# Optimization experiments

Hardware: AMD Instinct MI355X
Metric: run time of the kernel (lower is better)

Reference implementation:

```python
import jax, jax.numpy as jnp
import numpy as np

# --- config (matches init_kwargs) ---
E = 32          # n_routed_experts
G = 8           # n_group
TKG = 4         # topk_group
K = 4           # num_experts_per_tok
D = 2048        # hidden_size
H = 1024        # moe_intermediate_size
HS = 4096       # moe_shared_expert_intermediate_size
SCALE = 2.5     # routed_scaling_factor
CAP = 1024


def setup_inputs() -> dict:
    key = jax.random.key(0)
    ks = jax.random.split(key, 6)
    B, S = 2, 2048
    return dict(
        hidden_states=jax.random.normal(ks[0], (B, S, D), jnp.float32),
        gate_w=jax.random.normal(ks[1], (E, D), jnp.float32) * 0.02,
        bias_corr=jnp.zeros((E,), jnp.float32),  # e_score_correction_bias
        up_w=jax.random.normal(ks[2], (E, H, D), jnp.float32) * 0.02,
        down_w=jax.random.normal(ks[3], (E, D, H), jnp.float32) * 0.02,
        shared_up_w=jax.random.normal(ks[4], (HS, D), jnp.float32) * 0.02,
        shared_down_w=jax.random.normal(ks[5], (D, HS), jnp.float32) * 0.02,
    )


def relu2(x):
    r = jnp.maximum(x, 0.0)
    return r * r


def route_tokens(scores, bias_corr):
    # scores: sigmoid(router_logits), [T, E]
    T = scores.shape[0]
    scores_c = scores + bias_corr                                  # for choice
    group_scores = jax.lax.top_k(scores_c.reshape(T, G, E // G), 2)[0].sum(-1)  # [T, G]
    _, group_idx = jax.lax.top_k(group_scores, TKG)                # [T, TKG]
    group_mask = jnp.zeros((T, G), scores.dtype).at[jnp.arange(T)[:, None], group_idx].set(1.0)
    score_mask = jnp.repeat(group_mask, E // G, axis=1)            # [T, E]
    masked = jnp.where(score_mask > 0, scores_c, 0.0)
    _, topk_idx = jax.lax.top_k(masked, K)                         # [T, K]
    topk_w = jnp.take_along_axis(scores, topk_idx, axis=1)         # weights from raw sigmoid scores
    topk_w = topk_w / (topk_w.sum(-1, keepdims=True) + 1e-20)      # norm_topk_prob
    return topk_idx, topk_w * SCALE


def reference(hidden_states, gate_w, bias_corr, up_w, down_w, shared_up_w, shared_down_w):
    B, S, _ = hidden_states.shape
    T = B * S
    flat = hidden_states.reshape(T, D)

    logits = flat @ gate_w.T                                       # [T, E]
    scores = jax.nn.sigmoid(logits)
    topk_idx, topk_w = route_tokens(scores, bias_corr)             # [T, K] each

    # --- capacity-based dispatch (equivalent to per-expert gather + index_add combine) ---
    e_flat = topk_idx.reshape(-1)                                  # [T*K]
    oh = jax.nn.one_hot(e_flat, E, dtype=jnp.int32)                # [T*K, E]
    pos = jnp.take_along_axis(jnp.cumsum(oh, axis=0) - 1, e_flat[:, None], axis=1)[:, 0]
    tok = jnp.repeat(jnp.arange(T), K)                             # token idx per assignment
    valid = pos < CAP

    xe = jnp.zeros((E, CAP, D), flat.dtype).at[e_flat, pos].set(flat[tok], mode='drop')
    h = relu2(jnp.einsum('ecd,ehd->ech', xe, up_w))                # [E, CAP, H]
    ye = jnp.einsum('ech,edh->ecd', h, down_w)                     # [E, CAP, D]

    gathered = ye[e_flat, jnp.minimum(pos, CAP - 1)]               # [T*K, D]
    gathered = jnp.where(valid[:, None], gathered, 0.0) * topk_w.reshape(-1)[:, None]
    routed = gathered.reshape(T, K, D).sum(axis=1).reshape(B, S, D)

    shared = relu2(hidden_states @ shared_up_w.T) @ shared_down_w.T
    return routed + shared
```

## Files before the change

### kernel.cpp

```cpp
#include <hip/hip_runtime.h>

#define NE 32
#define NG 8
#define NK 4
#define ND 2048
#define NH 1024
#define NHS 4096
#define CAPE 1024
#define NT 4096

typedef float f32x4 __attribute__((ext_vector_type(4)));
typedef short s16x8 __attribute__((ext_vector_type(8)));

__device__ __forceinline__ short f2bf(float f) {
    return __builtin_bit_cast(short, (__bf16)f);
}
__device__ __forceinline__ float bf2f(short h) {
    return __builtin_bit_cast(float, ((unsigned)(unsigned short)h) << 16);
}

__device__ __forceinline__ void gload_lds16(const void* g, void* l) {
    __builtin_amdgcn_global_load_lds(
        (const __attribute__((address_space(1))) void*)g,
        (__attribute__((address_space(3))) void*)l, 16, 0, 0);
}

__global__ __launch_bounds__(256) void gate_kernel(
    const float* __restrict__ X, const float* __restrict__ Gw,
    const float* __restrict__ bias,
    int* __restrict__ topk_idx, float* __restrict__ topk_w)
{
    const int lane = threadIdx.x & 63;
    const int t = blockIdx.x * 4 + (threadIdx.x >> 6);
    const float* x = X + (size_t)t * ND;

    float xr[32];
#pragma unroll
    for (int i = 0; i < 32; i++) xr[i] = x[lane + i * 64];

    float scores[32];
#pragma unroll
    for (int e = 0; e < 32; e++) {
        const float* w = Gw + (size_t)e * ND;
        float a = 0.f;
#pragma unroll
        for (int i = 0; i < 32; i++) a = fmaf(xr[i], w[lane + i * 64], a);
#pragma unroll
        for (int s = 32; s > 0; s >>= 1) a += __shfl_xor(a, s);
        scores[e] = 1.0f / (1.0f + expf(-a));
    }

    float sc_c[32];
#pragma unroll
    for (int e = 0; e < 32; e++) sc_c[e] = scores[e] + bias[e];

    float gs[8];
#pragma unroll
    for (int g = 0; g < 8; g++) {
        float a = sc_c[4 * g], b = sc_c[4 * g + 1], c = sc_c[4 * g + 2], d = sc_c[4 * g + 3];
        float hi1 = fmaxf(a, b), lo1 = fminf(a, b);
        float hi2 = fmaxf(c, d), lo2 = fminf(c, d);
        float m1 = fmaxf(hi1, hi2);
        float m2 = fmaxf(fminf(hi1, hi2), fmaxf(lo1, lo2));
        gs[g] = m1 + m2;
    }

    unsigned gsel = 0;
#pragma unroll
    for (int it = 0; it < 4; it++) {
        int best = -1; float bv = -1e30f;
#pragma unroll
        for (int g = 0; g < 8; g++) {
            bool avail = !((gsel >> g) & 1);
            if (avail && gs[g] > bv) { bv = gs[g]; best = g; }
        }
        gsel |= 1u << best;
    }

    unsigned esel = 0;
    int idxs[4]; float wts[4];
#pragma unroll
    for (int it = 0; it < 4; it++) {
        int best = -1; float bv = -1e30f, braw = 0.f;
#pragma unroll
        for (int e = 0; e < 32; e++) {
            float mv = ((gsel >> (e >> 2)) & 1) ? sc_c[e] : 0.0f;
            bool avail = !((esel >> e) & 1);
            if (avail && mv > bv) { bv = mv; best = e; braw = scores[e]; }
        }
        esel |= 1u << best;
        idxs[it] = best; wts[it] = braw;
    }

    float s = wts[0] + wts[1] + wts[2] + wts[3] + 1e-20f;
    if (lane == 0) {
#pragma unroll
        for (int k = 0; k < 4; k++) {
            topk_idx[t * 4 + k] = idxs[k];
            topk_w[t * 4 + k] = wts[k] / s * 2.5f;
        }
    }
}

__global__ void zero_cnt(int* cnt) {
    if (threadIdx.x < NE) cnt[threadIdx.x] = 0;
}

__global__ void dispatch_kernel(const int* __restrict__ topk_idx,
                                int* __restrict__ cnt,
                                int* __restrict__ tok_list,
                                int* __restrict__ pos_list)
{
    int i = blockIdx.x * 256 + threadIdx.x;
    int e = topk_idx[i];
    int t = i >> 2;
    int pos = atomicAdd(&cnt[e], 1);
    pos_list[i] = pos;
    if (pos < CAPE) {
        tok_list[e * CAPE + pos] = t;
    }
}

__global__ __launch_bounds__(256) void cvt_f2bf(const float* __restrict__ in,
                                                short* __restrict__ out, int n8)
{
    int i = blockIdx.x * 256 + threadIdx.x;
    int stride = gridDim.x * 256;
    for (; i < n8; i += stride) {
        const f32x4* p = (const f32x4*)(in + (size_t)i * 8);
        f32x4 a = p[0], b = p[1];
        s16x8 h;
        h[0] = f2bf(a[0]); h[1] = f2bf(a[1]); h[2] = f2bf(a[2]); h[3] = f2bf(a[3]);
        h[4] = f2bf(b[0]); h[5] = f2bf(b[1]); h[6] = f2bf(b[2]); h[7] = f2bf(b[3]);
        *(s16x8*)(out + (size_t)i * 8) = h;
    }
}

__global__ __launch_bounds__(256) void combine_kernel(
    const int* __restrict__ topk_idx, const float* __restrict__ topk_w,
    const int* __restrict__ pos_list,
    const short* __restrict__ Ybuf, float* __restrict__ out)
{
    const int t = blockIdx.x;
    const int d0 = threadIdx.x * 8;

    int e[NK], p[NK]; float w[NK];
#pragma unroll
    for (int k = 0; k < NK; k++) {
        e[k] = topk_idx[t * NK + k];
        p[k] = pos_list[t * NK + k];
        w[k] = topk_w[t * NK + k];
    }

    float* orow = out + (size_t)t * ND + d0;
    f32x4 o0 = *(f32x4*)(orow);
    f32x4 o1 = *(f32x4*)(orow + 4);

#pragma unroll
    for (int k = 0; k < NK; k++) {
        if (p[k] < CAPE) {
            s16x8 y = *(const s16x8*)(Ybuf + ((size_t)e[k] * CAPE + p[k]) * ND + d0);
            o0[0] = fmaf(w[k], bf2f(y[0]), o0[0]);
            o0[1] = fmaf(w[k], bf2f(y[1]), o0[1]);
            o0[2] = fmaf(w[k], bf2f(y[2]), o0[2]);
            o0[3] = fmaf(w[k], bf2f(y[3]), o0[3]);
            o1[0] = fmaf(w[k], bf2f(y[4]), o1[0]);
            o1[1] = fmaf(w[k], bf2f(y[5]), o1[1]);
            o1[2] = fmaf(w[k], bf2f(y[6]), o1[2]);
            o1[3] = fmaf(w[k], bf2f(y[7]), o1[3]);
        }
    }
    *(f32x4*)(orow) = o0;
    *(f32x4*)(orow + 4) = o1;
}

template <int MODE>
__global__ __launch_bounds__(256, 2) void moe_gemm4(
    const short* __restrict__ Abase, const short* __restrict__ Bbase,
    const int* __restrict__ cnt, const int* __restrict__ tok_list,
    short* __restrict__ Hout, float* __restrict__ out)
{
    constexpr int K = (MODE == 0) ? ND : (MODE == 1) ? NH : (MODE == 2) ? ND : NHS;
    constexpr int NTILES = K / 64;

    const int e = blockIdx.z;
    const int m0 = blockIdx.y * 128, n0 = blockIdx.x * 128;

    int mcnt = 0;
    if constexpr (MODE == 0 || MODE == 1) {
        mcnt = min(cnt[e], CAPE);
        if (m0 >= mcnt) return;
    }

    __shared__ short As[2][128 * 64];
    __shared__ short Bs[2][128 * 64];

    const int tid = threadIdx.x;
    const int lane = tid & 63;
    const int wave = tid >> 6;
    const int wr = wave >> 1, wc = wave & 1;

    const short* Ab = Abase;
    const short* Bb = Bbase;
    if constexpr (MODE == 0) Bb += (size_t)e * NH * ND;
    if constexpr (MODE == 1) { Ab += (size_t)e * CAPE * NH; Bb += (size_t)e * ND * NH; }

    const int srow = tid >> 3;
    const int p = tid & 7;
    const int gcol = (p ^ (srow & 7)) * 8;
    const short* asrc[4];
    const short* bsrc[4];
    int dstoff[4];
#pragma unroll
    for (int o = 0; o < 4; o++) {
        int r = o * 32 + srow;
        if constexpr (MODE == 0) {
            int gr = min(m0 + r, mcnt - 1);
            int tok = tok_list[e * CAPE + gr];
            asrc[o] = Abase + (size_t)tok * ND + gcol;
        } else if constexpr (MODE == 1) {
            int gr = min(m0 + r, mcnt - 1);
            asrc[o] = Ab + (size_t)gr * NH + gcol;
        } else if constexpr (MODE == 2) {
            asrc[o] = Abase + (size_t)(m0 + r) * ND + gcol;
        } else {
            asrc[o] = Abase + (size_t)(m0 + r) * NHS + gcol;
        }
        bsrc[o] = Bb + (size_t)(n0 + o * 32 + srow) * K + gcol;
        dstoff[o] = o * 2048 + wave * 512;
    }

    auto STAGE = [&](int tt) {
        const int ko = (tt < NTILES ? tt : NTILES - 1) * 64;
        short* Ad = As[tt & 1];
        short* Bd = Bs[tt & 1];
#pragma unroll
        for (int o = 0; o < 4; o++) gload_lds16(asrc[o] + ko, Ad + dstoff[o]);
#pragma unroll
        for (int o = 0; o < 4; o++) gload_lds16(bsrc[o] + ko, Bd + dstoff[o]);
    };

    const int r16 = lane & 15;
    const int physbase = ((lane >> 4) ^ (lane & 7)) * 8;
    int offA[4], offB[4];
#pragma unroll
    for (int m = 0; m < 4; m++)
        offA[m] = (wr * 64 + m * 16 + r16) * 64 + physbase;
#pragma unroll
    for (int n = 0; n < 4; n++)
        offB[n] = (wc * 64 + n * 16 + r16) * 64 + physbase;

    f32x4 acc[4][4] = {};

    STAGE(0);
    STAGE(1);

    for (int t = 0; t < NTILES; ++t) {
        const short* At = As[t & 1];
        const short* Bt = Bs[t & 1];
        asm volatile("s_waitcnt vmcnt(8)" ::: "memory");
        __builtin_amdgcn_s_barrier();
        __builtin_amdgcn_sched_barrier(0);
        s16x8 af[4], bf[4];
#pragma unroll
        for (int m = 0; m < 4; m++) af[m] = *(const s16x8*)(At + offA[m]);
#pragma unroll
        for (int n = 0; n < 4; n++) bf[n] = *(const s16x8*)(Bt + offB[n]);
        asm volatile("s_waitcnt lgkmcnt(0)" ::: "memory");
        __builtin_amdgcn_sched_barrier(0);
        __builtin_amdgcn_s_setprio(1);
#pragma unroll
        for (int m = 0; m < 4; m++)
#pragma unroll
            for (int n = 0; n < 4; n++)
                acc[m][n] = __builtin_amdgcn_mfma_f32_16x16x32_bf16(af[m], bf[n], acc[m][n], 0, 0, 0);
        __builtin_amdgcn_s_setprio(0);
        s16x8 ag[4], bg[4];
#pragma unroll
        for (int m = 0; m < 4; m++) ag[m] = *(const s16x8*)(At + (offA[m] ^ 32));
#pragma unroll
        for (int n = 0; n < 4; n++) bg[n] = *(const s16x8*)(Bt + (offB[n] ^ 32));
        asm volatile("s_waitcnt lgkmcnt(0)" ::: "memory");
        __builtin_amdgcn_sched_barrier(0);
        __builtin_amdgcn_s_barrier();
        __builtin_amdgcn_sched_barrier(0);
        STAGE(t + 2);
        __builtin_amdgcn_s_setprio(1);
#pragma unroll
        for (int m = 0; m < 4; m++)
#pragma unroll
            for (int n = 0; n < 4; n++)
                acc[m][n] = __builtin_amdgcn_mfma_f32_16x16x32_bf16(ag[m], bg[n], acc[m][n], 0, 0, 0);
        __builtin_amdgcn_s_setprio(0);
    }

    const int r0 = (lane >> 4) * 4;
    const int cc = lane & 15;

    if constexpr (MODE == 0 || MODE == 2) {
#pragma unroll
        for (int i = 0; i < 4; i++)
#pragma unroll
            for (int j = 0; j < 4; j++)
#pragma unroll
                for (int v = 0; v < 4; v++) {
                    int row = wr * 64 + i * 16 + r0 + v;
                    int col = wc * 64 + j * 16 + cc;
                    float val = acc[i][j][v];
                    float r = fmaxf(val, 0.f);
                    val = r * r;
                    if constexpr (MODE == 0)
                        Hout[((size_t)e * CAPE + m0 + row) * NH + (n0 + col)] = f2bf(val);
                    else
                        Hout[(size_t)(m0 + row) * NHS + (n0 + col)] = f2bf(val);
                }
    } else if constexpr (MODE == 3) {
#pragma unroll
        for (int i = 0; i < 4; i++)
#pragma unroll
            for (int j = 0; j < 4; j++)
#pragma unroll
                for (int v = 0; v < 4; v++) {
                    int row = wr * 64 + i * 16 + r0 + v;
                    int col = wc * 64 + j * 16 + cc;
                    out[(size_t)(m0 + row) * ND + (n0 + col)] = acc[i][j][v];
                }
    } else {
#pragma unroll
        for (int i = 0; i < 4; i++)
#pragma unroll
            for (int v = 0; v < 4; v++) {
                int row = wr * 64 + i * 16 + r0 + v;
                int grow = m0 + row;
                if (grow < mcnt) {
#pragma unroll
                    for (int j = 0; j < 4; j++) {
                        int col = wc * 64 + j * 16 + cc;
                        Hout[((size_t)e * CAPE + grow) * ND + (n0 + col)] = f2bf(acc[i][j][v]);
                    }
                }
            }
    }
}

extern "C" void kernel_launch(void* const* d_in, const int* in_sizes, int n_in,
                              void* d_out, int out_size, void* d_ws, size_t ws_size,
                              hipStream_t stream) {
    const float* X    = (const float*)d_in[0];
    const float* Gw   = (const float*)d_in[1];
    const float* bias = (const float*)d_in[2];
    const float* up_w = (const float*)d_in[3];
    const float* dn_w = (const float*)d_in[4];
    const float* sup  = (const float*)d_in[5];
    const float* sdn  = (const float*)d_in[6];
    float* out = (float*)d_out;

    char* ws = (char*)d_ws;
    size_t off = 0;
    auto alloc = [&](size_t bytes) -> void* {
        off = (off + 255) & ~(size_t)255;
        void* p = ws + off;
        off += bytes;
        return p;
    };
    int*   cnt      = (int*)  alloc(NE * 4);
    int*   topk_idx = (int*)  alloc((size_t)NT * NK * 4);
    float* topk_w   = (float*)alloc((size_t)NT * NK * 4);
    int*   pos_list = (int*)  alloc((size_t)NT * NK * 4);
    int*   tok_list = (int*)  alloc((size_t)NE * CAPE * 4);
    short* Hbuf     = (short*)alloc((size_t)NE * CAPE * NH * 2);
    short* Sbuf     = (short*)alloc((size_t)NT * NHS * 2);
    short* Xbf      = (short*)alloc((size_t)NT * ND * 2);
    short* up_bf    = (short*)alloc((size_t)NE * NH * ND * 2);
    short* dn_bf    = (short*)alloc((size_t)NE * ND * NH * 2);
    short* sup_bf   = (short*)alloc((size_t)NHS * ND * 2);
    short* sdn_bf   = (short*)alloc((size_t)ND * NHS * 2);
    short* Ybuf     = Xbf;

    gate_kernel<<<dim3(NT / 4), dim3(256), 0, stream>>>(X, Gw, bias, topk_idx, topk_w);
    zero_cnt<<<dim3(1), dim3(64), 0, stream>>>(cnt);
    dispatch_kernel<<<dim3(NT * NK / 256), dim3(256), 0, stream>>>(
        topk_idx, cnt, tok_list, pos_list);

    cvt_f2bf<<<dim3(1024), dim3(256), 0, stream>>>(X,    Xbf,    NT * ND / 8);
    cvt_f2bf<<<dim3(2048), dim3(256), 0, stream>>>(up_w, up_bf,  NE * NH * ND / 8);
    cvt_f2bf<<<dim3(2048), dim3(256), 0, stream>>>(dn_w, dn_bf,  NE * ND * NH / 8);
    cvt_f2bf<<<dim3(1024), dim3(256), 0, stream>>>(sup,  sup_bf, NHS * ND / 8);
    cvt_f2bf<<<dim3(1024), dim3(256), 0, stream>>>(sdn,  sdn_bf, ND * NHS / 8);

    moe_gemm4<0><<<dim3(NH / 128, CAPE / 128, NE), dim3(256), 0, stream>>>(
        Xbf, up_bf, cnt, tok_list, Hbuf, nullptr);
    moe_gemm4<2><<<dim3(NHS / 128, NT / 128, 1), dim3(256), 0, stream>>>(
        Xbf, sup_bf, nullptr, nullptr, Sbuf, nullptr);
    moe_gemm4<3><<<dim3(ND / 128, NT / 128, 1), dim3(256), 0, stream>>>(
        Sbuf, sdn_bf, nullptr, nullptr, nullptr, out);
    moe_gemm4<1><<<dim3(ND / 128, CAPE / 128, NE), dim3(256), 0, stream>>>(
        Hbuf, dn_bf, cnt, tok_list, Ybuf, nullptr);
    combine_kernel<<<dim3(NT), dim3(256), 0, stream>>>(
        topk_idx, topk_w, pos_list, Ybuf, out);
}
```

Measured before the change: 678.5 us.

## Fuse fp32-to-bf16 weight conversion into GEMM B-tile loading

Removes the separate weight conversion kernels and has each GEMM load fp32 weight tiles through registers, converting to bf16 and writing them swizzled into LDS. The loop is unrolled by two with register double-buffering of B and prefetching three tiles ahead. This removes a large read/write pass over all weights, at the cost of doubled per-tile B traffic, extra VGPRs, and losing direct global-to-LDS loads for B. Ybuf now gets its own workspace instead of aliasing the bf16 X buffer.

Measured after the change: 645.0 us. 1.05x faster.

```diff
diff --git a/kernel.cpp b/kernel.cpp
--- a/kernel.cpp
+++ b/kernel.cpp
@@ -176,7 +176,7 @@
 
 template <int MODE>
 __global__ __launch_bounds__(256, 2) void moe_gemm4(
-    const short* __restrict__ Abase, const short* __restrict__ Bbase,
+    const short* __restrict__ Abase, const float* __restrict__ Bbase,
     const int* __restrict__ cnt, const int* __restrict__ tok_list,
     short* __restrict__ Hout, float* __restrict__ out)
 {
@@ -201,43 +201,65 @@
     const int wr = wave >> 1, wc = wave & 1;
 
     const short* Ab = Abase;
-    const short* Bb = Bbase;
+    const float* Bb = Bbase;
     if constexpr (MODE == 0) Bb += (size_t)e * NH * ND;
     if constexpr (MODE == 1) { Ab += (size_t)e * CAPE * NH; Bb += (size_t)e * ND * NH; }
 
     const int srow = tid >> 3;
-    const int p = tid & 7;
-    const int gcol = (p ^ (srow & 7)) * 8;
+    const int pA = tid & 7;
+    const int gcolA = (pA ^ (srow & 7)) * 8;
     const short* asrc[4];
-    const short* bsrc[4];
-    int dstoff[4];
+    int dstA[4];
 #pragma unroll
     for (int o = 0; o < 4; o++) {
         int r = o * 32 + srow;
         if constexpr (MODE == 0) {
             int gr = min(m0 + r, mcnt - 1);
             int tok = tok_list[e * CAPE + gr];
-            asrc[o] = Abase + (size_t)tok * ND + gcol;
+            asrc[o] = Abase + (size_t)tok * ND + gcolA;
         } else if constexpr (MODE == 1) {
             int gr = min(m0 + r, mcnt - 1);
-            asrc[o] = Ab + (size_t)gr * NH + gcol;
+            asrc[o] = Ab + (size_t)gr * NH + gcolA;
         } else if constexpr (MODE == 2) {
-            asrc[o] = Abase + (size_t)(m0 + r) * ND + gcol;
+            asrc[o] = Abase + (size_t)(m0 + r) * ND + gcolA;
         } else {
-            asrc[o] = Abase + (size_t)(m0 + r) * NHS + gcol;
-        }
-        bsrc[o] = Bb + (size_t)(n0 + o * 32 + srow) * K + gcol;
-        dstoff[o] = o * 2048 + wave * 512;
-    }
-
-    auto STAGE = [&](int tt) {
+            asrc[o] = Abase + (size_t)(m0 + r) * NHS + gcolA;
+        }
+        dstA[o] = o * 2048 + wave * 512;
+    }
+
+    const int brow = tid >> 4;
+    const int lc = tid & 15;
+    const float* bsrc[8];
+    int bdst[8];
+#pragma unroll
+    for (int o = 0; o < 8; o++) {
+        int r = o * 16 + brow;
+        bsrc[o] = Bb + (size_t)(n0 + r) * K + lc * 4;
+        int ks = lc >> 1;
+        bdst[o] = r * 64 + ((ks ^ (r & 7)) * 8) + (lc & 1) * 4;
+    }
+
+    auto STAGE_A = [&](int tt, int par) {
         const int ko = (tt < NTILES ? tt : NTILES - 1) * 64;
-        short* Ad = As[tt & 1];
-        short* Bd = Bs[tt & 1];
-#pragma unroll
-        for (int o = 0; o < 4; o++) gload_lds16(asrc[o] + ko, Ad + dstoff[o]);
-#pragma unroll
-        for (int o = 0; o < 4; o++) gload_lds16(bsrc[o] + ko, Bd + dstoff[o]);
+        short* Ad = As[par];
+#pragma unroll
+        for (int o = 0; o < 4; o++) gload_lds16(asrc[o] + ko, Ad + dstA[o]);
+    };
+    auto BLOAD = [&](int tt, f32x4* regs) {
+        const int ko = (tt < NTILES ? tt : NTILES - 1) * 64;
+#pragma unroll
+        for (int o = 0; o < 8; o++) regs[o] = *(const f32x4*)(bsrc[o] + ko);
+    };
+    auto BWRITE = [&](const f32x4* regs, int par) {
+        short* Bd = Bs[par];
+#pragma unroll
+        for (int o = 0; o < 8; o++) {
+            short4 h;
+            h.x = f2bf(regs[o][0]); h.y = f2bf(regs[o][1]);
+            h.z = f2bf(regs[o][2]); h.w = f2bf(regs[o][3]);
+            *(short4*)(Bd + bdst[o]) = h;
+        }
     };
 
     const int r16 = lane & 15;
@@ -251,48 +273,72 @@
         offB[n] = (wc * 64 + n * 16 + r16) * 64 + physbase;
 
     f32x4 acc[4][4] = {};
-
-    STAGE(0);
-    STAGE(1);
-
-    for (int t = 0; t < NTILES; ++t) {
-        const short* At = As[t & 1];
-        const short* Bt = Bs[t & 1];
-        asm volatile("s_waitcnt vmcnt(8)" ::: "memory");
-        __builtin_amdgcn_s_barrier();
-        __builtin_amdgcn_sched_barrier(0);
-        s16x8 af[4], bf[4];
-#pragma unroll
-        for (int m = 0; m < 4; m++) af[m] = *(const s16x8*)(At + offA[m]);
-#pragma unroll
-        for (int n = 0; n < 4; n++) bf[n] = *(const s16x8*)(Bt + offB[n]);
-        asm volatile("s_waitcnt lgkmcnt(0)" ::: "memory");
-        __builtin_amdgcn_sched_barrier(0);
-        __builtin_amdgcn_s_setprio(1);
-#pragma unroll
-        for (int m = 0; m < 4; m++)
-#pragma unroll
-            for (int n = 0; n < 4; n++)
-                acc[m][n] = __builtin_amdgcn_mfma_f32_16x16x32_bf16(af[m], bf[n], acc[m][n], 0, 0, 0);
-        __builtin_amdgcn_s_setprio(0);
-        s16x8 ag[4], bg[4];
-#pragma unroll
-        for (int m = 0; m < 4; m++) ag[m] = *(const s16x8*)(At + (offA[m] ^ 32));
-#pragma unroll
-        for (int n = 0; n < 4; n++) bg[n] = *(const s16x8*)(Bt + (offB[n] ^ 32));
-        asm volatile("s_waitcnt lgkmcnt(0)" ::: "memory");
-        __builtin_amdgcn_sched_barrier(0);
-        __builtin_amdgcn_s_barrier();
-        __builtin_amdgcn_sched_barrier(0);
-        STAGE(t + 2);
-        __builtin_amdgcn_s_setprio(1);
-#pragma unroll
-        for (int m = 0; m < 4; m++)
-#pragma unroll
-            for (int n = 0; n < 4; n++)
-                acc[m][n] = __builtin_amdgcn_mfma_f32_16x16x32_bf16(ag[m], bg[n], acc[m][n], 0, 0, 0);
-        __builtin_amdgcn_s_setprio(0);
-    }
+    f32x4 brE[8], brO[8];
+
+    STAGE_A(0, 0); STAGE_A(1, 1);
+    BLOAD(0, brE); BLOAD(1, brO);
+    asm volatile("s_waitcnt vmcnt(8)" ::: "memory");
+    __builtin_amdgcn_sched_barrier(0);
+    BWRITE(brE, 0);
+    asm volatile("s_waitcnt vmcnt(0)" ::: "memory");
+    __builtin_amdgcn_sched_barrier(0);
+    BWRITE(brO, 1);
+    BLOAD(2, brE);
+    asm volatile("s_waitcnt lgkmcnt(0)" ::: "memory");
+    __builtin_amdgcn_sched_barrier(0);
+
+#define GEMM_ITER(T, PAR, CONSUME, FILL)                                        \
+    {                                                                           \
+        __builtin_amdgcn_s_barrier();                                           \
+        __builtin_amdgcn_sched_barrier(0);                                      \
+        const short* At = As[PAR];                                              \
+        const short* Bt = Bs[PAR];                                              \
+        s16x8 af[4], bf[4];                                                     \
+        _Pragma("unroll")                                                       \
+        for (int m = 0; m < 4; m++) af[m] = *(const s16x8*)(At + offA[m]);      \
+        _Pragma("unroll")                                                       \
+        for (int n = 0; n < 4; n++) bf[n] = *(const s16x8*)(Bt + offB[n]);      \
+        asm volatile("s_waitcnt lgkmcnt(0)" ::: "memory");                      \
+        __builtin_amdgcn_sched_barrier(0);                                      \
+        __builtin_amdgcn_s_setprio(1);                                          \
+        _Pragma("unroll")                                                       \
+        for (int m = 0; m < 4; m++)                                             \
+            _Pragma("unroll")                                                   \
+            for (int n = 0; n < 4; n++)                                         \
+                acc[m][n] = __builtin_amdgcn_mfma_f32_16x16x32_bf16(            \
+                    af[m], bf[n], acc[m][n], 0, 0, 0);                          \
+        __builtin_amdgcn_s_setprio(0);                                          \
+        s16x8 ag[4], bg[4];                                                     \
+        _Pragma("unroll")                                                       \
+        for (int m = 0; m < 4; m++) ag[m] = *(const s16x8*)(At + (offA[m] ^ 32)); \
+        _Pragma("unroll")                                                       \
+        for (int n = 0; n < 4; n++) bg[n] = *(const s16x8*)(Bt + (offB[n] ^ 32)); \
+        asm volatile("s_waitcnt lgkmcnt(0)" ::: "memory");                      \
+        __builtin_amdgcn_sched_barrier(0);                                      \
+        __builtin_amdgcn_s_barrier();         \
+        __builtin_amdgcn_sched_barrier(0);                                      \
+        STAGE_A((T) + 2, PAR);                                                  \
+        BLOAD((T) + 3, FILL);                                                   \
+        asm volatile("s_waitcnt vmcnt(12)" ::: "memory");  \
+        __builtin_amdgcn_sched_barrier(0);                                      \
+        BWRITE(CONSUME, PAR);                                                   \
+        __builtin_amdgcn_s_setprio(1);                                          \
+        _Pragma("unroll")                                                       \
+        for (int m = 0; m < 4; m++)                                             \
+            _Pragma("unroll")                                                   \
+            for (int n = 0; n < 4; n++)                                         \
+                acc[m][n] = __builtin_amdgcn_mfma_f32_16x16x32_bf16(            \
+                    ag[m], bg[n], acc[m][n], 0, 0, 0);                          \
+        __builtin_amdgcn_s_setprio(0);                                          \
+        asm volatile("s_waitcnt lgkmcnt(0)" ::: "memory");                      \
+        __builtin_amdgcn_sched_barrier(0);                                      \
+    }
+
+    for (int t = 0; t < NTILES; t += 2) {
+        GEMM_ITER(t,     0, brE, brO);
+        GEMM_ITER(t + 1, 1, brO, brE);
+    }
+#undef GEMM_ITER
 
     const int r0 = (lane >> 4) * 4;
     const int cc = lane & 15;
@@ -371,31 +417,23 @@
     short* Hbuf     = (short*)alloc((size_t)NE * CAPE * NH * 2);
     short* Sbuf     = (short*)alloc((size_t)NT * NHS * 2);
     short* Xbf      = (short*)alloc((size_t)NT * ND * 2);
-    short* up_bf    = (short*)alloc((size_t)NE * NH * ND * 2);
-    short* dn_bf    = (short*)alloc((size_t)NE * ND * NH * 2);
-    short* sup_bf   = (short*)alloc((size_t)NHS * ND * 2);
-    short* sdn_bf   = (short*)alloc((size_t)ND * NHS * 2);
-    short* Ybuf     = Xbf;
+    short* Ybuf     = (short*)alloc((size_t)NE * CAPE * ND * 2);
 
     gate_kernel<<<dim3(NT / 4), dim3(256), 0, stream>>>(X, Gw, bias, topk_idx, topk_w);
     zero_cnt<<<dim3(1), dim3(64), 0, stream>>>(cnt);
     dispatch_kernel<<<dim3(NT * NK / 256), dim3(256), 0, stream>>>(
         topk_idx, cnt, tok_list, pos_list);
 
-    cvt_f2bf<<<dim3(1024), dim3(256), 0, stream>>>(X,    Xbf,    NT * ND / 8);
-    cvt_f2bf<<<dim3(2048), dim3(256), 0, stream>>>(up_w, up_bf,  NE * NH * ND / 8);
-    cvt_f2bf<<<dim3(2048), dim3(256), 0, stream>>>(dn_w, dn_bf,  NE * ND * NH / 8);
-    cvt_f2bf<<<dim3(1024), dim3(256), 0, stream>>>(sup,  sup_bf, NHS * ND / 8);
-    cvt_f2bf<<<dim3(1024), dim3(256), 0, stream>>>(sdn,  sdn_bf, ND * NHS / 8);
+    cvt_f2bf<<<dim3(1024), dim3(256), 0, stream>>>(X, Xbf, NT * ND / 8);
 
     moe_gemm4<0><<<dim3(NH / 128, CAPE / 128, NE), dim3(256), 0, stream>>>(
-        Xbf, up_bf, cnt, tok_list, Hbuf, nullptr);
+        Xbf, up_w, cnt, tok_list, Hbuf, nullptr);
     moe_gemm4<2><<<dim3(NHS / 128, NT / 128, 1), dim3(256), 0, stream>>>(
-        Xbf, sup_bf, nullptr, nullptr, Sbuf, nullptr);
+        Xbf, sup, nullptr, nullptr, Sbuf, nullptr);
     moe_gemm4<3><<<dim3(ND / 128, NT / 128, 1), dim3(256), 0, stream>>>(
-        Sbuf, sdn_bf, nullptr, nullptr, nullptr, out);
+        Sbuf, sdn, nullptr, nullptr, nullptr, out);
     moe_gemm4<1><<<dim3(ND / 128, CAPE / 128, NE), dim3(256), 0, stream>>>(
-        Hbuf, dn_bf, cnt, tok_list, Ybuf, nullptr);
+        Hbuf, dn_w, cnt, tok_list, Ybuf, nullptr);
     combine_kernel<<<dim3(NT), dim3(256), 0, stream>>>(
         topk_idx, topk_w, pos_list, Ybuf, out);
 }
```
